# Kernel tuning notes

Measured on AMD Instinct MI355X. Metric: run time of the kernel, lower is better.

## Reference

```python
import jax, jax.numpy as jnp
import numpy as np

S, N_PER, N_FEAT, HID = 4, 12500, 1024, 256
N_STRUCT = 500


def setup_inputs() -> dict:
    key = jax.random.key(0)
    ks = jax.random.split(key, 11)
    sc = 1.0 / np.sqrt(N_FEAT)
    sh = 1.0 / np.sqrt(HID)
    return {
        "features": jax.random.normal(ks[0], (S, N_PER, N_FEAT), jnp.float32),
        "W1": jax.random.normal(ks[1], (S, N_FEAT, HID), jnp.float32) * sc,
        "b1": jax.random.normal(ks[2], (S, HID), jnp.float32) * 0.01,
        "W2": jax.random.normal(ks[3], (S, HID, HID), jnp.float32) * sh,
        "b2": jax.random.normal(ks[4], (S, HID), jnp.float32) * 0.01,
        "W3": jax.random.normal(ks[5], (S, HID, HID), jnp.float32) * sh,
        "b3": jax.random.normal(ks[6], (S, HID), jnp.float32) * 0.01,
        "W4": jax.random.normal(ks[7], (S, HID, 1), jnp.float32) * sh,
        "b4": jax.random.normal(ks[8], (S, 1), jnp.float32) * 0.01,
        "structure_idx": jax.random.randint(ks[9], (S, N_PER), 0, N_STRUCT, jnp.int64 if jax.config.jax_enable_x64 else jnp.int32).astype(jnp.int32),
        "n_structures": N_STRUCT,
    }


def reference(features, W1, b1, W2, b2, W3, b3, W4, b4, structure_idx, n_structures):
    # Per-species 4-layer SiLU MLP applied to species-grouped feature blocks.
    h = jax.nn.silu(jnp.einsum("snf,sfh->snh", features, W1) + b1[:, None, :])
    h = jax.nn.silu(jnp.einsum("snh,shk->snk", h, W2) + b2[:, None, :])
    h = jax.nn.silu(jnp.einsum("snh,shk->snk", h, W3) + b3[:, None, :])
    e = jnp.einsum("snh,sho->sno", h, W4) + b4[:, None, :]  # [S, N_per, 1]
    atomic_energies = e[..., 0].reshape(-1)                  # concat over species
    # index_add_ into per-structure energies
    energies = jax.ops.segment_sum(atomic_energies, structure_idx.reshape(-1), num_segments=n_structures)
    return energies
```

## Files before the change

### kernel.cpp

```cpp
#include <hip/hip_runtime.h>

typedef _Float16 f16;
typedef __attribute__((ext_vector_type(8))) _Float16 f16x8;
typedef __attribute__((ext_vector_type(4))) float f32x4;
typedef unsigned int u32;

#define S_      4
#define NPER    12500
#define NF      1024
#define HID     256
#define NSTRUCT 500
#define TM      64

#define GLB __attribute__((address_space(1)))
#define AS3 __attribute__((address_space(3)))

#define WAIT_VM(N)  asm volatile("s_waitcnt vmcnt(" #N ")" ::: "memory")
#define WAIT_LGKM() asm volatile("s_waitcnt lgkmcnt(0)" ::: "memory")
#define SCHED0()    __builtin_amdgcn_sched_barrier(0)
#define BARRIER()   do { __builtin_amdgcn_s_barrier(); SCHED0(); } while (0)

__global__ __launch_bounds__(256) void transpose_all_kernel(
    const float* __restrict__ W1, const float* __restrict__ W2,
    const float* __restrict__ W3,
    f16* __restrict__ w1t, f16* __restrict__ w2t, f16* __restrict__ w3t)
{
  const int z = blockIdx.z;
  const int layer = z >> 2, sp = z & 3;
  const float* in; f16* out; int K;
  if (layer == 0)      { in = W1; out = w1t; K = NF;  }
  else if (layer == 1) { in = W2; out = w2t; K = HID; }
  else                 { in = W3; out = w3t; K = HID; }
  if (blockIdx.x * 64 >= K) return;

  __shared__ float tile[64][65];
  const float* inp = in + (size_t)sp * K * HID;
  f16* outp = out + (size_t)sp * K * HID;
  const int k0 = blockIdx.x * 64;
  const int n0 = blockIdx.y * 64;
  const int t = threadIdx.x;
  {
    const int lk = t >> 2;
    const int nq = (t & 3) * 16;
    const float* src = inp + (size_t)(k0 + lk) * HID + n0 + nq;
    #pragma unroll
    for (int i = 0; i < 4; ++i) {
      float4 v = *(const float4*)(src + i * 4);
      tile[lk][nq + i * 4 + 0] = v.x;
      tile[lk][nq + i * 4 + 1] = v.y;
      tile[lk][nq + i * 4 + 2] = v.z;
      tile[lk][nq + i * 4 + 3] = v.w;
    }
  }
  __syncthreads();
  {
    const int ln = t >> 2;
    const int kq = (t & 3) * 16;
    f16* dst = outp + (size_t)(n0 + ln) * K + k0 + kq;
    f16x8 a, b;
    #pragma unroll
    for (int j = 0; j < 8; ++j) a[j] = (f16)tile[kq + j][ln];
    #pragma unroll
    for (int j = 0; j < 8; ++j) b[j] = (f16)tile[kq + 8 + j][ln];
    *(f16x8*)dst = a;
    *(f16x8*)(dst + 8) = b;
  }
}


__device__ __forceinline__ void zero_acc(f32x4 (&acc)[4][4]) {
  #pragma unroll
  for (int a = 0; a < 4; ++a)
    #pragma unroll
    for (int b = 0; b < 4; ++b)
      #pragma unroll
      for (int j = 0; j < 4; ++j) acc[a][b][j] = 0.f;
}

__device__ __forceinline__ void stage_w64(char* bS, const char* wbase, int c,
                                          int w, int lane)
{
  #pragma unroll
  for (int i = 0; i < 8; ++i) {
    const int seg  = w * 8 + i;
    const int rloc = lane >> 3;
    const int p    = lane & 7;
    const int row  = seg * 8 + rloc;
    const int slog = p ^ rloc;
    const char* gp = wbase + (size_t)row * (NF * 2) + (size_t)c * 128 + slog * 16;
    char* lp = bS + seg * 1024;
    __builtin_amdgcn_global_load_lds((const GLB u32*)gp, (AS3 u32*)lp, 16, 0, 0);
  }
}

__device__ __forceinline__ void stage_w32(char* wS, const char* wbase, int c,
                                          int w, int lane)
{
  #pragma unroll
  for (int i = 0; i < 4; ++i) {
    const int seg = w * 4 + i;
    const int row = seg * 16 + (lane >> 2);
    const int kbp = lane & 3;
    const int kb  = kbp ^ ((row >> 1) & 3);
    const char* gp = wbase + (size_t)row * (HID * 2) + c * 64 + kb * 16;
    char* lp = wS + seg * 1024;
    __builtin_amdgcn_global_load_lds((const GLB u32*)gp, (AS3 u32*)lp, 16, 0, 0);
  }
}

__device__ __forceinline__ void load_pa(float4 (&pa)[4], const float* fsrcT, int c)
{
  #pragma unroll
  for (int j = 0; j < 4; ++j)
    pa[j] = *(const float4*)(fsrcT + c * 64 + j * 4);
}

__device__ __forceinline__ void stage_feat64(char* aS, const float4 (&pa)[4], int t)
{
  const int r = t >> 2;
  #pragma unroll
  for (int wr = 0; wr < 2; ++wr) {
    f16x8 hv;
    const float4 lo = pa[wr * 2 + 0], hi = pa[wr * 2 + 1];
    hv[0]=(f16)lo.x; hv[1]=(f16)lo.y; hv[2]=(f16)lo.z; hv[3]=(f16)lo.w;
    hv[4]=(f16)hi.x; hv[5]=(f16)hi.y; hv[6]=(f16)hi.z; hv[7]=(f16)hi.w;
    const int slog = (t & 3) * 2 + wr;
    const int p = slog ^ (r & 7);
    *(f16x8*)(aS + r * 128 + p * 16) = hv;
  }
}

__device__ __forceinline__ void mfma64_a(f32x4 (&acc)[4][4], const char* aS,
                                         const char* bS, int w, int g, int l15)
{
  #pragma unroll
  for (int ks = 0; ks < 2; ++ks) {
    f16x8 af[4], bf[4];
    #pragma unroll
    for (int at = 0; at < 4; ++at) {
      const int rr = at * 16 + l15;
      const int p  = (ks * 4 + g) ^ (rr & 7);
      af[at] = *(const f16x8*)(aS + rr * 128 + p * 16);
    }
    #pragma unroll
    for (int bt = 0; bt < 4; ++bt) {
      const int nn = w * 64 + bt * 16 + l15;
      const int p  = (ks * 4 + g) ^ (nn & 7);
      bf[bt] = *(const f16x8*)(bS + nn * 128 + p * 16);
    }
    #pragma unroll
    for (int at = 0; at < 4; ++at)
      #pragma unroll
      for (int bt = 0; bt < 4; ++bt)
        acc[at][bt] = __builtin_amdgcn_mfma_f32_16x16x32_f16(af[at], bf[bt], acc[at][bt], 0, 0, 0);
  }
}

__device__ __forceinline__ void mfma32_h(f32x4 (&acc)[4][4], const char* hL, int c,
                                         const char* wS, int w, int g, int l15)
{
  f16x8 af[4], bf[4];
  #pragma unroll
  for (int at = 0; at < 4; ++at) {
    const int rr = at * 16 + l15;
    af[at] = *(const f16x8*)(hL + ((rr * 512 + c * 64 + g * 16) ^ ((rr & 7) << 4)));
  }
  #pragma unroll
  for (int bt = 0; bt < 4; ++bt) {
    const int nn = w * 64 + bt * 16 + l15;
    bf[bt] = *(const f16x8*)(wS + nn * 64 + ((g ^ ((nn >> 1) & 3)) * 16));
  }
  #pragma unroll
  for (int at = 0; at < 4; ++at)
    #pragma unroll
    for (int bt = 0; bt < 4; ++bt)
      acc[at][bt] = __builtin_amdgcn_mfma_f32_16x16x32_f16(af[at], bf[bt], acc[at][bt], 0, 0, 0);
}

__device__ __forceinline__ void silu_store(f32x4 (&acc)[4][4],
                                           const float* __restrict__ bias,
                                           char* hL, int w, int lane)
{
  const int g = lane >> 4, l15 = lane & 15;
  #pragma unroll
  for (int bt = 0; bt < 4; ++bt) {
    const int col = w * 64 + bt * 16 + l15;
    const float b = bias[col];
    #pragma unroll
    for (int at = 0; at < 4; ++at) {
      #pragma unroll
      for (int j = 0; j < 4; ++j) {
        const int row = at * 16 + g * 4 + j;
        float x = acc[at][bt][j] + b;
        x = x * __builtin_amdgcn_rcpf(1.f + __expf(-x));
        *(f16*)(hL + (((row * HID + col) * 2) ^ ((row & 7) << 4))) = (f16)x;
      }
    }
  }
}

#define L1_STEP(c, ASc, ASn, BSc, BSn, PAset, VMN, DOF, DOG, DOPA)  \
  do {                                                               \
    if (DOF)  stage_feat64(ASn, PAset, t);                           \
    if (DOG)  stage_w64(BSn, w1s, (c) + 1, w, lane);                 \
    if (DOPA) load_pa(PAset, fsrcT, (c) + 3);                        \
    WAIT_VM(VMN); SCHED0();                                          \
    mfma64_a(acc, ASc, BSc, w, g, l15);                              \
    WAIT_LGKM(); BARRIER();                                          \
  } while (0)

#define HID_NB(c, WSc, WSn, wsrc, DOG)                               \
  do {                                                               \
    WAIT_LGKM(); SCHED0();                                           \
    if (DOG) stage_w32(WSn, wsrc, (c) + 1, w, lane);                 \
    WAIT_VM(4); SCHED0();                                            \
    mfma32_h(acc, hL, c, WSc, w, g, l15);                            \
  } while (0)

__global__ __launch_bounds__(256, 2) void mlp_fused_kernel(
    const float* __restrict__ feats,
    const float* __restrict__ b1g,
    const float* __restrict__ b2g,
    const float* __restrict__ b3g,
    const float* __restrict__ w4g,
    const float* __restrict__ b4g,
    const int*   __restrict__ sidxg,
    const f16*   __restrict__ w1t,
    const f16*   __restrict__ w2t,
    const f16*   __restrict__ w3t,
    float*       __restrict__ outg)
{
  __shared__ char arena[80 * 1024];
  char* aS0 = arena;
  char* aS1 = arena + 8 * 1024;
  char* bS0 = arena + 16 * 1024;
  char* bS1 = arena + 48 * 1024;
  char* hL  = arena;
  char* wS0 = arena + 32 * 1024;
  char* wS1 = arena + 48 * 1024;

  const int s    = blockIdx.y;
  const int row0 = blockIdx.x * TM;
  const int t    = threadIdx.x;
  const int lane = t & 63;
  const int w    = t >> 6;
  const int g    = lane >> 4;
  const int l15  = lane & 15;

  const int gr   = row0 + (t >> 2);
  const bool valid = gr < NPER;
  const int grc  = valid ? gr : (NPER - 1);
  const float* fsrcT = feats + ((size_t)s * NPER + grc) * NF + (t & 3) * 16;
  const char*  w1s   = (const char*)(w1t + (size_t)s * HID * NF);
  const char*  w2s   = (const char*)(w2t + (size_t)s * HID * HID);
  const char*  w3s   = (const char*)(w3t + (size_t)s * HID * HID);

  f32x4 acc[4][4];
  zero_acc(acc);

  float4 pf[4], paA[4], paB[4];
  load_pa(pf, fsrcT, 0);
  stage_w64(bS0, w1s, 0, w, lane);
  load_pa(paA, fsrcT, 1);
  load_pa(paB, fsrcT, 2);
  stage_feat64(aS0, pf, t);
  WAIT_LGKM(); BARRIER();

  L1_STEP(0, aS0, aS1, bS0, bS1, paA, 20, 1, 1, 1);
  for (int cc = 1; cc <= 11; cc += 2) {
    L1_STEP(cc,     aS1, aS0, bS1, bS0, paB, 16, 1, 1, 1);
    L1_STEP(cc + 1, aS0, aS1, bS0, bS1, paA, 16, 1, 1, 1);
  }
  L1_STEP(13, aS1, aS0, bS1, bS0, paB, 12, 1, 1, 0);
  L1_STEP(14, aS0, aS1, bS0, bS1, paA,  8, 1, 1, 0);
  {
    stage_w32(wS0, w2s, 0, w, lane);
    WAIT_VM(4); SCHED0();
    mfma64_a(acc, aS1, bS1, w, g, l15);
    WAIT_LGKM(); BARRIER();
  }

  silu_store(acc, b1g + s * HID, hL, w, lane);
  zero_acc(acc);
  WAIT_LGKM(); BARRIER();

  HID_NB(0, wS0, wS1, w2s, 1);
  HID_NB(1, wS1, wS0, w2s, 1);
  HID_NB(2, wS0, wS1, w2s, 1);
  HID_NB(3, wS1, wS0, w2s, 1);
  HID_NB(4, wS0, wS1, w2s, 1);
  HID_NB(5, wS1, wS0, w2s, 1);
  HID_NB(6, wS0, wS1, w2s, 1);
  {
    WAIT_LGKM(); SCHED0();
    stage_w32(wS0, w3s, 0, w, lane);
    WAIT_VM(4); SCHED0();
    mfma32_h(acc, hL, 7, wS1, w, g, l15);
  }
  BARRIER();
  silu_store(acc, b2g + s * HID, hL, w, lane);
  zero_acc(acc);
  WAIT_LGKM(); BARRIER();

  HID_NB(0, wS0, wS1, w3s, 1);
  HID_NB(1, wS1, wS0, w3s, 1);
  HID_NB(2, wS0, wS1, w3s, 1);
  HID_NB(3, wS1, wS0, w3s, 1);
  HID_NB(4, wS0, wS1, w3s, 1);
  HID_NB(5, wS1, wS0, w3s, 1);
  HID_NB(6, wS0, wS1, w3s, 1);
  {
    WAIT_VM(0); SCHED0();
    mfma32_h(acc, hL, 7, wS1, w, g, l15);
  }
  BARRIER();
  silu_store(acc, b3g + s * HID, hL, w, lane);
  WAIT_LGKM(); BARRIER();

  {
    const int row = t >> 2;
    const int q   = t & 3;
    const float* w4 = w4g + s * HID;
    float sum = 0.f;
    #pragma unroll
    for (int j8 = 0; j8 < 64; j8 += 8) {
      const int k = q * 64 + j8;
      f16x8 hv = *(const f16x8*)(hL + (((row * HID + k) * 2) ^ ((row & 7) << 4)));
      float4 wa = *(const float4*)(w4 + k);
      float4 wb = *(const float4*)(w4 + k + 4);
      sum += (float)hv[0] * wa.x + (float)hv[1] * wa.y + (float)hv[2] * wa.z + (float)hv[3] * wa.w
           + (float)hv[4] * wb.x + (float)hv[5] * wb.y + (float)hv[6] * wb.z + (float)hv[7] * wb.w;
    }
    sum += __shfl_xor(sum, 1);
    sum += __shfl_xor(sum, 2);
    if (q == 0 && valid) {
      atomicAdd(&outg[sidxg[s * NPER + gr]], sum + b4g[s]);
    }
  }
}

extern "C" void kernel_launch(void* const* d_in, const int* in_sizes, int n_in,
                              void* d_out, int out_size, void* d_ws, size_t ws_size,
                              hipStream_t stream)
{
  const float* feats = (const float*)d_in[0];
  const float* W1    = (const float*)d_in[1];
  const float* b1    = (const float*)d_in[2];
  const float* W2    = (const float*)d_in[3];
  const float* b2    = (const float*)d_in[4];
  const float* W3    = (const float*)d_in[5];
  const float* b3    = (const float*)d_in[6];
  const float* W4    = (const float*)d_in[7];
  const float* b4    = (const float*)d_in[8];
  const int*   sidx  = (const int*)d_in[9];
  float* out = (float*)d_out;

  f16* w1t = (f16*)d_ws;
  f16* w2t = w1t + (size_t)S_ * HID * NF;
  f16* w3t = w2t + (size_t)S_ * HID * HID;

  hipMemsetAsync(d_out, 0, NSTRUCT * sizeof(float), stream);
  transpose_all_kernel<<<dim3(16, 4, 12), 256, 0, stream>>>(W1, W2, W3, w1t, w2t, w3t);
  mlp_fused_kernel<<<dim3((NPER + TM - 1) / TM, S_), 256, 0, stream>>>(
      feats, b1, b2, b3, W4, b4, sidx, w1t, w2t, w3t, out);
}
```

Before: 110.1 us.

## Stage fp32 features via direct LDS loads and keep weight tiles in registers

Features are now copied straight from global memory into LDS as fp32 with async global_load_lds into a triple buffer, and converted to fp16 only when the MFMA operands are read. Weight tiles for all three layers are loaded from global memory directly into registers, double-buffered, instead of being staged in LDS. This shrinks LDS from 80KB to 48KB so three blocks can share a CU, and removes the register round-trip and conversion stores for features. In exchange, LDS traffic per feature element doubles, register pressure rises, and the hidden layers issue global weight loads without explicit waits, relying on the compiler to insert them.

```diff
diff --git a/kernel.cpp b/kernel.cpp
--- a/kernel.cpp
+++ b/kernel.cpp
@@ -77,104 +77,76 @@
       for (int j = 0; j < 4; ++j) acc[a][b][j] = 0.f;
 }
 
-__device__ __forceinline__ void stage_w64(char* bS, const char* wbase, int c,
-                                          int w, int lane)
-{
-  #pragma unroll
-  for (int i = 0; i < 8; ++i) {
-    const int seg  = w * 8 + i;
-    const int rloc = lane >> 3;
-    const int p    = lane & 7;
-    const int row  = seg * 8 + rloc;
-    const int slog = p ^ rloc;
-    const char* gp = wbase + (size_t)row * (NF * 2) + (size_t)c * 128 + slog * 16;
-    char* lp = bS + seg * 1024;
+__device__ __forceinline__ void stage_a64(char* aS, const float* fbase, int c,
+                                          int row0, int w, int lane)
+{
+  #pragma unroll
+  for (int i = 0; i < 4; ++i) {
+    const int row  = i * 16 + w * 4 + (lane >> 4);
+    const int p    = lane & 15;
+    const int slog = p ^ (row & 15);
+    int rg = row0 + row; if (rg > NPER - 1) rg = NPER - 1;
+    const float* gp = fbase + (size_t)rg * NF + c * 64 + slog * 4;
+    char* lp = aS + ((i * 16 + w * 4) << 8);
     __builtin_amdgcn_global_load_lds((const GLB u32*)gp, (AS3 u32*)lp, 16, 0, 0);
   }
 }
 
-__device__ __forceinline__ void stage_w32(char* wS, const char* wbase, int c,
-                                          int w, int lane)
-{
-  #pragma unroll
-  for (int i = 0; i < 4; ++i) {
-    const int seg = w * 4 + i;
-    const int row = seg * 16 + (lane >> 2);
-    const int kbp = lane & 3;
-    const int kb  = kbp ^ ((row >> 1) & 3);
-    const char* gp = wbase + (size_t)row * (HID * 2) + c * 64 + kb * 16;
-    char* lp = wS + seg * 1024;
-    __builtin_amdgcn_global_load_lds((const GLB u32*)gp, (AS3 u32*)lp, 16, 0, 0);
-  }
-}
-
-__device__ __forceinline__ void load_pa(float4 (&pa)[4], const float* fsrcT, int c)
-{
-  #pragma unroll
-  for (int j = 0; j < 4; ++j)
-    pa[j] = *(const float4*)(fsrcT + c * 64 + j * 4);
-}
-
-__device__ __forceinline__ void stage_feat64(char* aS, const float4 (&pa)[4], int t)
-{
-  const int r = t >> 2;
-  #pragma unroll
-  for (int wr = 0; wr < 2; ++wr) {
-    f16x8 hv;
-    const float4 lo = pa[wr * 2 + 0], hi = pa[wr * 2 + 1];
-    hv[0]=(f16)lo.x; hv[1]=(f16)lo.y; hv[2]=(f16)lo.z; hv[3]=(f16)lo.w;
-    hv[4]=(f16)hi.x; hv[5]=(f16)hi.y; hv[6]=(f16)hi.z; hv[7]=(f16)hi.w;
-    const int slog = (t & 3) * 2 + wr;
-    const int p = slog ^ (r & 7);
-    *(f16x8*)(aS + r * 128 + p * 16) = hv;
-  }
-}
-
-__device__ __forceinline__ void mfma64_a(f32x4 (&acc)[4][4], const char* aS,
-                                         const char* bS, int w, int g, int l15)
+__device__ __forceinline__ void load_b64(f16x8 (&bf)[8], const f16* wsrc, int c,
+                                         int K, int w, int g, int l15)
+{
+  #pragma unroll
+  for (int ks = 0; ks < 2; ++ks)
+    #pragma unroll
+    for (int bt = 0; bt < 4; ++bt) {
+      const int nn = w * 64 + bt * 16 + l15;
+      bf[ks * 4 + bt] = *(const f16x8*)(wsrc + (size_t)nn * K + c * 64 + (ks * 4 + g) * 8);
+    }
+}
+
+__device__ __forceinline__ void mfma64_f32a(f32x4 (&acc)[4][4], const char* aS,
+                                            const f16x8 (&bf)[8], int g, int l15)
 {
   #pragma unroll
   for (int ks = 0; ks < 2; ++ks) {
-    f16x8 af[4], bf[4];
+    f16x8 af[4];
     #pragma unroll
     for (int at = 0; at < 4; ++at) {
       const int rr = at * 16 + l15;
-      const int p  = (ks * 4 + g) ^ (rr & 7);
-      af[at] = *(const f16x8*)(aS + rr * 128 + p * 16);
-    }
-    #pragma unroll
-    for (int bt = 0; bt < 4; ++bt) {
-      const int nn = w * 64 + bt * 16 + l15;
-      const int p  = (ks * 4 + g) ^ (nn & 7);
-      bf[bt] = *(const f16x8*)(bS + nn * 128 + p * 16);
+      const int sw = rr & 15;
+      const int s0 = ks * 8 + g * 2;
+      const f32x4 lo = *(const f32x4*)(aS + rr * 256 + ((s0    ) ^ sw) * 16);
+      const f32x4 hi = *(const f32x4*)(aS + rr * 256 + ((s0 + 1) ^ sw) * 16);
+      f16x8 a;
+      a[0]=(f16)lo[0]; a[1]=(f16)lo[1]; a[2]=(f16)lo[2]; a[3]=(f16)lo[3];
+      a[4]=(f16)hi[0]; a[5]=(f16)hi[1]; a[6]=(f16)hi[2]; a[7]=(f16)hi[3];
+      af[at] = a;
     }
     #pragma unroll
     for (int at = 0; at < 4; ++at)
       #pragma unroll
       for (int bt = 0; bt < 4; ++bt)
-        acc[at][bt] = __builtin_amdgcn_mfma_f32_16x16x32_f16(af[at], bf[bt], acc[at][bt], 0, 0, 0);
-  }
-}
-
-__device__ __forceinline__ void mfma32_h(f32x4 (&acc)[4][4], const char* hL, int c,
-                                         const char* wS, int w, int g, int l15)
-{
-  f16x8 af[4], bf[4];
-  #pragma unroll
-  for (int at = 0; at < 4; ++at) {
-    const int rr = at * 16 + l15;
-    af[at] = *(const f16x8*)(hL + ((rr * 512 + c * 64 + g * 16) ^ ((rr & 7) << 4)));
-  }
-  #pragma unroll
-  for (int bt = 0; bt < 4; ++bt) {
-    const int nn = w * 64 + bt * 16 + l15;
-    bf[bt] = *(const f16x8*)(wS + nn * 64 + ((g ^ ((nn >> 1) & 3)) * 16));
-  }
-  #pragma unroll
-  for (int at = 0; at < 4; ++at)
-    #pragma unroll
-    for (int bt = 0; bt < 4; ++bt)
-      acc[at][bt] = __builtin_amdgcn_mfma_f32_16x16x32_f16(af[at], bf[bt], acc[at][bt], 0, 0, 0);
+        acc[at][bt] = __builtin_amdgcn_mfma_f32_16x16x32_f16(af[at], bf[ks*4+bt], acc[at][bt], 0, 0, 0);
+  }
+}
+
+__device__ __forceinline__ void mfma64_h(f32x4 (&acc)[4][4], const char* hL, int cH,
+                                         const f16x8 (&bf)[8], int g, int l15)
+{
+  #pragma unroll
+  for (int ks = 0; ks < 2; ++ks) {
+    f16x8 af[4];
+    #pragma unroll
+    for (int at = 0; at < 4; ++at) {
+      const int rr = at * 16 + l15;
+      af[at] = *(const f16x8*)(hL + ((rr * 512 + cH * 128 + ks * 64 + g * 16) ^ ((rr & 7) << 4)));
+    }
+    #pragma unroll
+    for (int at = 0; at < 4; ++at)
+      #pragma unroll
+      for (int bt = 0; bt < 4; ++bt)
+        acc[at][bt] = __builtin_amdgcn_mfma_f32_16x16x32_f16(af[at], bf[ks*4+bt], acc[at][bt], 0, 0, 0);
+  }
 }
 
 __device__ __forceinline__ void silu_store(f32x4 (&acc)[4][4],
@@ -199,25 +171,16 @@
   }
 }
 
-#define L1_STEP(c, ASc, ASn, BSc, BSn, PAset, VMN, DOF, DOG, DOPA)  \
-  do {                                                               \
-    if (DOF)  stage_feat64(ASn, PAset, t);                           \
-    if (DOG)  stage_w64(BSn, w1s, (c) + 1, w, lane);                 \
-    if (DOPA) load_pa(PAset, fsrcT, (c) + 3);                        \
-    WAIT_VM(VMN); SCHED0();                                          \
-    mfma64_a(acc, ASc, BSc, w, g, l15);                              \
-    WAIT_LGKM(); BARRIER();                                          \
+#define L1_PH(c, AScur, ASstg, BFcur, BFnxt, DOA, DOB, VMN)   \
+  do {                                                         \
+    if (DOA) stage_a64(ASstg, fbase, (c) + 2, row0, w, lane);  \
+    if (DOB) load_b64(BFnxt, w1s, (c) + 1, NF, w, g, l15);     \
+    WAIT_VM(VMN); SCHED0();                                    \
+    mfma64_f32a(acc, AScur, BFcur, g, l15);                    \
+    WAIT_LGKM(); BARRIER();                                    \
   } while (0)
 
-#define HID_NB(c, WSc, WSn, wsrc, DOG)                               \
-  do {                                                               \
-    WAIT_LGKM(); SCHED0();                                           \
-    if (DOG) stage_w32(WSn, wsrc, (c) + 1, w, lane);                 \
-    WAIT_VM(4); SCHED0();                                            \
-    mfma32_h(acc, hL, c, WSc, w, g, l15);                            \
-  } while (0)
-
-__global__ __launch_bounds__(256, 2) void mlp_fused_kernel(
+__global__ __launch_bounds__(256, 3) void mlp_fused_kernel(
     const float* __restrict__ feats,
     const float* __restrict__ b1g,
     const float* __restrict__ b2g,
@@ -230,14 +193,11 @@
     const f16*   __restrict__ w3t,
     float*       __restrict__ outg)
 {
-  __shared__ char arena[80 * 1024];
+  __shared__ char arena[48 * 1024];
   char* aS0 = arena;
-  char* aS1 = arena + 8 * 1024;
-  char* bS0 = arena + 16 * 1024;
-  char* bS1 = arena + 48 * 1024;
+  char* aS1 = arena + 16 * 1024;
+  char* aS2 = arena + 32 * 1024;
   char* hL  = arena;
-  char* wS0 = arena + 32 * 1024;
-  char* wS1 = arena + 48 * 1024;
 
   const int s    = blockIdx.y;
   const int row0 = blockIdx.x * TM;
@@ -250,33 +210,40 @@
   const int gr   = row0 + (t >> 2);
   const bool valid = gr < NPER;
   const int grc  = valid ? gr : (NPER - 1);
-  const float* fsrcT = feats + ((size_t)s * NPER + grc) * NF + (t & 3) * 16;
-  const char*  w1s   = (const char*)(w1t + (size_t)s * HID * NF);
-  const char*  w2s   = (const char*)(w2t + (size_t)s * HID * HID);
-  const char*  w3s   = (const char*)(w3t + (size_t)s * HID * HID);
+  const float* fbase = feats + (size_t)s * NPER * NF;
+  const f16*   w1s   = w1t + (size_t)s * HID * NF;
+  const f16*   w2s   = w2t + (size_t)s * HID * HID;
+  const f16*   w3s   = w3t + (size_t)s * HID * HID;
 
   f32x4 acc[4][4];
+  f16x8 bfA[8], bfB[8];
   zero_acc(acc);
 
-  float4 pf[4], paA[4], paB[4];
-  load_pa(pf, fsrcT, 0);
-  stage_w64(bS0, w1s, 0, w, lane);
-  load_pa(paA, fsrcT, 1);
-  load_pa(paB, fsrcT, 2);
-  stage_feat64(aS0, pf, t);
-  WAIT_LGKM(); BARRIER();
-
-  L1_STEP(0, aS0, aS1, bS0, bS1, paA, 20, 1, 1, 1);
-  for (int cc = 1; cc <= 11; cc += 2) {
-    L1_STEP(cc,     aS1, aS0, bS1, bS0, paB, 16, 1, 1, 1);
-    L1_STEP(cc + 1, aS0, aS1, bS0, bS1, paA, 16, 1, 1, 1);
-  }
-  L1_STEP(13, aS1, aS0, bS1, bS0, paB, 12, 1, 1, 0);
-  L1_STEP(14, aS0, aS1, bS0, bS1, paA,  8, 1, 1, 0);
+  stage_a64(aS0, fbase, 0, row0, w, lane);
+  stage_a64(aS1, fbase, 1, row0, w, lane);
+  load_b64(bfA, w1s, 0, NF, w, g, l15);
+  WAIT_VM(12); SCHED0();
+  BARRIER();
+
+  L1_PH(0,  aS0, aS2, bfA, bfB, 1, 1, 12);
+  L1_PH(1,  aS1, aS0, bfB, bfA, 1, 1, 12);
+  L1_PH(2,  aS2, aS1, bfA, bfB, 1, 1, 12);
+  L1_PH(3,  aS0, aS2, bfB, bfA, 1, 1, 12);
+  L1_PH(4,  aS1, aS0, bfA, bfB, 1, 1, 12);
+  L1_PH(5,  aS2, aS1, bfB, bfA, 1, 1, 12);
+  L1_PH(6,  aS0, aS2, bfA, bfB, 1, 1, 12);
+  L1_PH(7,  aS1, aS0, bfB, bfA, 1, 1, 12);
+  L1_PH(8,  aS2, aS1, bfA, bfB, 1, 1, 12);
+  L1_PH(9,  aS0, aS2, bfB, bfA, 1, 1, 12);
+  L1_PH(10, aS1, aS0, bfA, bfB, 1, 1, 12);
+  L1_PH(11, aS2, aS1, bfB, bfA, 1, 1, 12);
+  L1_PH(12, aS0, aS2, bfA, bfB, 1, 1, 12);
+  L1_PH(13, aS1, aS0, bfB, bfA, 1, 1, 12);
+  L1_PH(14, aS2, aS0, bfA, bfB, 0, 1, 8);
   {
-    stage_w32(wS0, w2s, 0, w, lane);
-    WAIT_VM(4); SCHED0();
-    mfma64_a(acc, aS1, bS1, w, g, l15);
+    WAIT_VM(0); SCHED0();
+    mfma64_f32a(acc, aS0, bfB, g, l15);
+    load_b64(bfA, w2s, 0, HID, w, g, l15);
     WAIT_LGKM(); BARRIER();
   }
 
@@ -284,35 +251,26 @@
   zero_acc(acc);
   WAIT_LGKM(); BARRIER();
 
-  HID_NB(0, wS0, wS1, w2s, 1);
-  HID_NB(1, wS1, wS0, w2s, 1);
-  HID_NB(2, wS0, wS1, w2s, 1);
-  HID_NB(3, wS1, wS0, w2s, 1);
-  HID_NB(4, wS0, wS1, w2s, 1);
-  HID_NB(5, wS1, wS0, w2s, 1);
-  HID_NB(6, wS0, wS1, w2s, 1);
-  {
-    WAIT_LGKM(); SCHED0();
-    stage_w32(wS0, w3s, 0, w, lane);
-    WAIT_VM(4); SCHED0();
-    mfma32_h(acc, hL, 7, wS1, w, g, l15);
-  }
+  load_b64(bfB, w2s, 1, HID, w, g, l15);
+  mfma64_h(acc, hL, 0, bfA, g, l15);
+  load_b64(bfA, w2s, 2, HID, w, g, l15);
+  mfma64_h(acc, hL, 1, bfB, g, l15);
+  load_b64(bfB, w2s, 3, HID, w, g, l15);
+  mfma64_h(acc, hL, 2, bfA, g, l15);
+  load_b64(bfA, w3s, 0, HID, w, g, l15);
+  mfma64_h(acc, hL, 3, bfB, g, l15);
   BARRIER();
   silu_store(acc, b2g + s * HID, hL, w, lane);
   zero_acc(acc);
   WAIT_LGKM(); BARRIER();
 
-  HID_NB(0, wS0, wS1, w3s, 1);
-  HID_NB(1, wS1, wS0, w3s, 1);
-  HID_NB(2, wS0, wS1, w3s, 1);
-  HID_NB(3, wS1, wS0, w3s, 1);
-  HID_NB(4, wS0, wS1, w3s, 1);
-  HID_NB(5, wS1, wS0, w3s, 1);
-  HID_NB(6, wS0, wS1, w3s, 1);
-  {
-    WAIT_VM(0); SCHED0();
-    mfma32_h(acc, hL, 7, wS1, w, g, l15);
-  }
+  load_b64(bfB, w3s, 1, HID, w, g, l15);
+  mfma64_h(acc, hL, 0, bfA, g, l15);
+  load_b64(bfA, w3s, 2, HID, w, g, l15);
+  mfma64_h(acc, hL, 1, bfB, g, l15);
+  load_b64(bfB, w3s, 3, HID, w, g, l15);
+  mfma64_h(acc, hL, 2, bfA, g, l15);
+  mfma64_h(acc, hL, 3, bfB, g, l15);
   BARRIER();
   silu_store(acc, b3g + s * HID, hL, w, lane);
   WAIT_LGKM(); BARRIER();
```

New measurement: 158.3 us. +43.8%, slower.

## Deepen prefetch pipelines: 4-stage feature loads and triple-buffered hidden weights

Applied to the files above, without the earlier changes.

Layer 1 now keeps three register prefetch sets for feature tiles, loading chunk c+4 instead of c+3, so global-load latency has more time to hide. The hidden layers switch from double to triple-buffered weight staging in LDS, using a third 16KB slot. The weights for layer 3 are prefetched across the layer boundary. This raises register pressure and keeps more loads in flight, and it relies on the per-wave waitcnt discipline staying correct without barriers between stages.

```diff
diff --git a/kernel.cpp b/kernel.cpp
--- a/kernel.cpp
+++ b/kernel.cpp
@@ -199,22 +199,22 @@
   }
 }
 
-#define L1_STEP(c, ASc, ASn, BSc, BSn, PAset, VMN, DOF, DOG, DOPA)  \
-  do {                                                               \
-    if (DOF)  stage_feat64(ASn, PAset, t);                           \
-    if (DOG)  stage_w64(BSn, w1s, (c) + 1, w, lane);                 \
-    if (DOPA) load_pa(PAset, fsrcT, (c) + 3);                        \
-    WAIT_VM(VMN); SCHED0();                                          \
-    mfma64_a(acc, ASc, BSc, w, g, l15);                              \
-    WAIT_LGKM(); BARRIER();                                          \
+#define L1_STEP(c, ASc, ASn, BSc, BSn, PAset, VMN, DOG, DOPA)   \
+  do {                                                           \
+    stage_feat64(ASn, PAset, t);                                 \
+    if (DOG)  stage_w64(BSn, w1s, (c) + 1, w, lane);             \
+    if (DOPA) load_pa(PAset, fsrcT, (c) + 4);                    \
+    WAIT_VM(VMN); SCHED0();                                      \
+    mfma64_a(acc, ASc, BSc, w, g, l15);                          \
+    WAIT_LGKM(); BARRIER();                                      \
   } while (0)
 
-#define HID_NB(c, WSc, WSn, wsrc, DOG)                               \
-  do {                                                               \
-    WAIT_LGKM(); SCHED0();                                           \
-    if (DOG) stage_w32(WSn, wsrc, (c) + 1, w, lane);                 \
-    WAIT_VM(4); SCHED0();                                            \
-    mfma32_h(acc, hL, c, WSc, w, g, l15);                            \
+#define HID_ST(c, WSc, WSstg, wsrc, cs)                          \
+  do {                                                           \
+    WAIT_VM(8); SCHED0();                                        \
+    mfma32_h(acc, hL, c, WSc, w, g, l15);                        \
+    WAIT_LGKM(); SCHED0();                                       \
+    stage_w32(WSstg, wsrc, cs, w, lane);                         \
   } while (0)
 
 __global__ __launch_bounds__(256, 2) void mlp_fused_kernel(
@@ -238,6 +238,7 @@
   char* hL  = arena;
   char* wS0 = arena + 32 * 1024;
   char* wS1 = arena + 48 * 1024;
+  char* wS2 = arena + 64 * 1024;
 
   const int s    = blockIdx.y;
   const int row0 = blockIdx.x * TM;
@@ -258,21 +259,30 @@
   f32x4 acc[4][4];
   zero_acc(acc);
 
-  float4 pf[4], paA[4], paB[4];
+  float4 pf[4], paA[4], paB[4], paC[4];
   load_pa(pf, fsrcT, 0);
   stage_w64(bS0, w1s, 0, w, lane);
   load_pa(paA, fsrcT, 1);
   load_pa(paB, fsrcT, 2);
+  load_pa(paC, fsrcT, 3);
   stage_feat64(aS0, pf, t);
   WAIT_LGKM(); BARRIER();
 
-  L1_STEP(0, aS0, aS1, bS0, bS1, paA, 20, 1, 1, 1);
-  for (int cc = 1; cc <= 11; cc += 2) {
-    L1_STEP(cc,     aS1, aS0, bS1, bS0, paB, 16, 1, 1, 1);
-    L1_STEP(cc + 1, aS0, aS1, bS0, bS1, paA, 16, 1, 1, 1);
-  }
-  L1_STEP(13, aS1, aS0, bS1, bS0, paB, 12, 1, 1, 0);
-  L1_STEP(14, aS0, aS1, bS0, bS1, paA,  8, 1, 1, 0);
+  L1_STEP(0,  aS0, aS1, bS0, bS1, paA, 20, 1, 1);
+  L1_STEP(1,  aS1, aS0, bS1, bS0, paB, 16, 1, 1);
+  L1_STEP(2,  aS0, aS1, bS0, bS1, paC, 16, 1, 1);
+  L1_STEP(3,  aS1, aS0, bS1, bS0, paA, 16, 1, 1);
+  L1_STEP(4,  aS0, aS1, bS0, bS1, paB, 16, 1, 1);
+  L1_STEP(5,  aS1, aS0, bS1, bS0, paC, 16, 1, 1);
+  L1_STEP(6,  aS0, aS1, bS0, bS1, paA, 16, 1, 1);
+  L1_STEP(7,  aS1, aS0, bS1, bS0, paB, 16, 1, 1);
+  L1_STEP(8,  aS0, aS1, bS0, bS1, paC, 16, 1, 1);
+  L1_STEP(9,  aS1, aS0, bS1, bS0, paA, 16, 1, 1);
+  L1_STEP(10, aS0, aS1, bS0, bS1, paB, 16, 1, 1);
+  L1_STEP(11, aS1, aS0, bS1, bS0, paC, 16, 1, 1);
+  L1_STEP(12, aS0, aS1, bS0, bS1, paA, 12, 1, 0);
+  L1_STEP(13, aS1, aS0, bS1, bS0, paB,  8, 1, 0);
+  L1_STEP(14, aS0, aS1, bS0, bS1, paC,  8, 1, 0);
   {
     stage_w32(wS0, w2s, 0, w, lane);
     WAIT_VM(4); SCHED0();
@@ -282,37 +292,31 @@
 
   silu_store(acc, b1g + s * HID, hL, w, lane);
   zero_acc(acc);
+  stage_w32(wS1, w2s, 1, w, lane);
+  stage_w32(wS2, w2s, 2, w, lane);
   WAIT_LGKM(); BARRIER();
 
-  HID_NB(0, wS0, wS1, w2s, 1);
-  HID_NB(1, wS1, wS0, w2s, 1);
-  HID_NB(2, wS0, wS1, w2s, 1);
-  HID_NB(3, wS1, wS0, w2s, 1);
-  HID_NB(4, wS0, wS1, w2s, 1);
-  HID_NB(5, wS1, wS0, w2s, 1);
-  HID_NB(6, wS0, wS1, w2s, 1);
-  {
-    WAIT_LGKM(); SCHED0();
-    stage_w32(wS0, w3s, 0, w, lane);
-    WAIT_VM(4); SCHED0();
-    mfma32_h(acc, hL, 7, wS1, w, g, l15);
-  }
+  HID_ST(0, wS0, wS0, w2s, 3);
+  HID_ST(1, wS1, wS1, w2s, 4);
+  HID_ST(2, wS2, wS2, w2s, 5);
+  HID_ST(3, wS0, wS0, w2s, 6);
+  HID_ST(4, wS1, wS1, w2s, 7);
+  HID_ST(5, wS2, wS2, w3s, 0);
+  HID_ST(6, wS0, wS0, w3s, 1);
+  HID_ST(7, wS1, wS1, w3s, 2);
   BARRIER();
   silu_store(acc, b2g + s * HID, hL, w, lane);
   zero_acc(acc);
   WAIT_LGKM(); BARRIER();
 
-  HID_NB(0, wS0, wS1, w3s, 1);
-  HID_NB(1, wS1, wS0, w3s, 1);
-  HID_NB(2, wS0, wS1, w3s, 1);
-  HID_NB(3, wS1, wS0, w3s, 1);
-  HID_NB(4, wS0, wS1, w3s, 1);
-  HID_NB(5, wS1, wS0, w3s, 1);
-  HID_NB(6, wS0, wS1, w3s, 1);
-  {
-    WAIT_VM(0); SCHED0();
-    mfma32_h(acc, hL, 7, wS1, w, g, l15);
-  }
+  HID_ST(0, wS2, wS2, w3s, 3);
+  HID_ST(1, wS0, wS0, w3s, 4);
+  HID_ST(2, wS1, wS1, w3s, 5);
+  HID_ST(3, wS2, wS2, w3s, 6);
+  HID_ST(4, wS0, wS0, w3s, 7);
+  { WAIT_VM(8); SCHED0(); mfma32_h(acc, hL, 5, wS1, w, g, l15); }
+  { WAIT_VM(4); SCHED0(); mfma32_h(acc, hL, 6, wS2, w, g, l15); }
+  { WAIT_VM(0); SCHED0(); mfma32_h(acc, hL, 7, wS0, w, g, l15); }
   BARRIER();
   silu_store(acc, b3g + s * HID, hL, w, lane);
   WAIT_LGKM(); BARRIER();
```

After: 108.3 us. No clear change (-1.6%).

## Enlarge row tile to 96 and restructure LDS pipeline with 4-deep feature ring

Applied to the files above, without the earlier changes.

Raises the per-block row tile from 64 to 96 so each staged weight chunk is reused across more rows, reducing weight traffic per row and block count. Layer 1 switches to a four-slot feature ring in LDS with a single weight buffer and a barrier every two steps. The hidden layers prefetch two weight chunks ahead, including across the layer boundary. More accumulator registers (6x4 tiles) may pressure occupancy at 2 blocks/CU, and the LDS reuse pattern relies on careful wait counts.

```diff
diff --git a/kernel.cpp b/kernel.cpp
--- a/kernel.cpp
+++ b/kernel.cpp
@@ -10,7 +10,7 @@
 #define NF      1024
 #define HID     256
 #define NSTRUCT 500
-#define TM      64
+#define TM      96
 
 #define GLB __attribute__((address_space(1)))
 #define AS3 __attribute__((address_space(3)))
@@ -68,9 +68,9 @@
 }
 
 
-__device__ __forceinline__ void zero_acc(f32x4 (&acc)[4][4]) {
-  #pragma unroll
-  for (int a = 0; a < 4; ++a)
+__device__ __forceinline__ void zero_acc(f32x4 (&acc)[6][4]) {
+  #pragma unroll
+  for (int a = 0; a < 6; ++a)
     #pragma unroll
     for (int b = 0; b < 4; ++b)
       #pragma unroll
@@ -108,36 +108,37 @@
   }
 }
 
-__device__ __forceinline__ void load_pa(float4 (&pa)[4], const float* fsrcT, int c)
-{
-  #pragma unroll
-  for (int j = 0; j < 4; ++j)
-    pa[j] = *(const float4*)(fsrcT + c * 64 + j * 4);
-}
-
-__device__ __forceinline__ void stage_feat64(char* aS, const float4 (&pa)[4], int t)
-{
-  const int r = t >> 2;
-  #pragma unroll
-  for (int wr = 0; wr < 2; ++wr) {
+__device__ __forceinline__ void load_pa96(float4 (&pa)[6],
+                                          const float* const (&agp)[3], int c)
+{
+  #pragma unroll
+  for (int i = 0; i < 3; ++i) {
+    pa[2*i]   = *(const float4*)(agp[i] + (size_t)c * 64);
+    pa[2*i+1] = *(const float4*)(agp[i] + (size_t)c * 64 + 4);
+  }
+}
+
+__device__ __forceinline__ void stage_feat96(char* aS, const float4 (&pa)[6],
+                                             const u32 (&aof)[3])
+{
+  #pragma unroll
+  for (int i = 0; i < 3; ++i) {
     f16x8 hv;
-    const float4 lo = pa[wr * 2 + 0], hi = pa[wr * 2 + 1];
+    const float4 lo = pa[2*i], hi = pa[2*i+1];
     hv[0]=(f16)lo.x; hv[1]=(f16)lo.y; hv[2]=(f16)lo.z; hv[3]=(f16)lo.w;
     hv[4]=(f16)hi.x; hv[5]=(f16)hi.y; hv[6]=(f16)hi.z; hv[7]=(f16)hi.w;
-    const int slog = (t & 3) * 2 + wr;
-    const int p = slog ^ (r & 7);
-    *(f16x8*)(aS + r * 128 + p * 16) = hv;
-  }
-}
-
-__device__ __forceinline__ void mfma64_a(f32x4 (&acc)[4][4], const char* aS,
+    *(f16x8*)(aS + aof[i]) = hv;
+  }
+}
+
+__device__ __forceinline__ void mfma96_a(f32x4 (&acc)[6][4], const char* aS,
                                          const char* bS, int w, int g, int l15)
 {
   #pragma unroll
   for (int ks = 0; ks < 2; ++ks) {
-    f16x8 af[4], bf[4];
-    #pragma unroll
-    for (int at = 0; at < 4; ++at) {
+    f16x8 af[6], bf[4];
+    #pragma unroll
+    for (int at = 0; at < 6; ++at) {
       const int rr = at * 16 + l15;
       const int p  = (ks * 4 + g) ^ (rr & 7);
       af[at] = *(const f16x8*)(aS + rr * 128 + p * 16);
@@ -149,19 +150,19 @@
       bf[bt] = *(const f16x8*)(bS + nn * 128 + p * 16);
     }
     #pragma unroll
-    for (int at = 0; at < 4; ++at)
+    for (int at = 0; at < 6; ++at)
       #pragma unroll
       for (int bt = 0; bt < 4; ++bt)
         acc[at][bt] = __builtin_amdgcn_mfma_f32_16x16x32_f16(af[at], bf[bt], acc[at][bt], 0, 0, 0);
   }
 }
 
-__device__ __forceinline__ void mfma32_h(f32x4 (&acc)[4][4], const char* hL, int c,
+__device__ __forceinline__ void mfma32_h(f32x4 (&acc)[6][4], const char* hL, int c,
                                          const char* wS, int w, int g, int l15)
 {
-  f16x8 af[4], bf[4];
-  #pragma unroll
-  for (int at = 0; at < 4; ++at) {
+  f16x8 af[6], bf[4];
+  #pragma unroll
+  for (int at = 0; at < 6; ++at) {
     const int rr = at * 16 + l15;
     af[at] = *(const f16x8*)(hL + ((rr * 512 + c * 64 + g * 16) ^ ((rr & 7) << 4)));
   }
@@ -171,13 +172,13 @@
     bf[bt] = *(const f16x8*)(wS + nn * 64 + ((g ^ ((nn >> 1) & 3)) * 16));
   }
   #pragma unroll
-  for (int at = 0; at < 4; ++at)
+  for (int at = 0; at < 6; ++at)
     #pragma unroll
     for (int bt = 0; bt < 4; ++bt)
       acc[at][bt] = __builtin_amdgcn_mfma_f32_16x16x32_f16(af[at], bf[bt], acc[at][bt], 0, 0, 0);
 }
 
-__device__ __forceinline__ void silu_store(f32x4 (&acc)[4][4],
+__device__ __forceinline__ void silu_store(f32x4 (&acc)[6][4],
                                            const float* __restrict__ bias,
                                            char* hL, int w, int lane)
 {
@@ -187,7 +188,7 @@
     const int col = w * 64 + bt * 16 + l15;
     const float b = bias[col];
     #pragma unroll
-    for (int at = 0; at < 4; ++at) {
+    for (int at = 0; at < 6; ++at) {
       #pragma unroll
       for (int j = 0; j < 4; ++j) {
         const int row = at * 16 + g * 4 + j;
@@ -199,22 +200,25 @@
   }
 }
 
-#define L1_STEP(c, ASc, ASn, BSc, BSn, PAset, VMN, DOF, DOG, DOPA)  \
-  do {                                                               \
-    if (DOF)  stage_feat64(ASn, PAset, t);                           \
-    if (DOG)  stage_w64(BSn, w1s, (c) + 1, w, lane);                 \
-    if (DOPA) load_pa(PAset, fsrcT, (c) + 3);                        \
-    WAIT_VM(VMN); SCHED0();                                          \
-    mfma64_a(acc, ASc, BSc, w, g, l15);                              \
-    WAIT_LGKM(); BARRIER();                                          \
+#define ASB(c) (arena + (((c) & 3) * 12288))
+
+#define L1_STEP(c, PAset, VMN, DOG, DOF, DOPA, DOBAR)              \
+  do {                                                             \
+    WAIT_VM(VMN); SCHED0();                                        \
+    mfma96_a(acc, ASB(c), bS, w, g, l15);                          \
+    WAIT_LGKM(); SCHED0();                                         \
+    if (DOG)  { stage_w64(bS, w1s, (c) + 1, w, lane); SCHED0(); }  \
+    if (DOF)  { stage_feat96(ASB((c) + 2), PAset, aof); SCHED0(); }\
+    if (DOPA) { load_pa96(PAset, agp, (c) + 4); SCHED0(); }        \
+    if (DOBAR) { WAIT_LGKM(); BARRIER(); }                         \
   } while (0)
 
-#define HID_NB(c, WSc, WSn, wsrc, DOG)                               \
-  do {                                                               \
-    WAIT_LGKM(); SCHED0();                                           \
-    if (DOG) stage_w32(WSn, wsrc, (c) + 1, w, lane);                 \
-    WAIT_VM(4); SCHED0();                                            \
-    mfma32_h(acc, hL, c, WSc, w, g, l15);                            \
+#define HID_ST(c, WH, wsrc, cs)                                  \
+  do {                                                           \
+    WAIT_VM(4); SCHED0();                                        \
+    mfma32_h(acc, hL, c, WH, w, g, l15);                         \
+    WAIT_LGKM(); SCHED0();                                       \
+    stage_w32(WH, wsrc, cs, w, lane); SCHED0();                  \
   } while (0)
 
 __global__ __launch_bounds__(256, 2) void mlp_fused_kernel(
@@ -231,13 +235,10 @@
     float*       __restrict__ outg)
 {
   __shared__ char arena[80 * 1024];
-  char* aS0 = arena;
-  char* aS1 = arena + 8 * 1024;
-  char* bS0 = arena + 16 * 1024;
-  char* bS1 = arena + 48 * 1024;
+  char* bS  = arena + 48 * 1024;
   char* hL  = arena;
-  char* wS0 = arena + 32 * 1024;
-  char* wS1 = arena + 48 * 1024;
+  char* wH0 = arena + 48 * 1024;
+  char* wH1 = arena + 64 * 1024;
 
   const int s    = blockIdx.y;
   const int row0 = blockIdx.x * TM;
@@ -247,94 +248,107 @@
   const int g    = lane >> 4;
   const int l15  = lane & 15;
 
-  const int gr   = row0 + (t >> 2);
-  const bool valid = gr < NPER;
-  const int grc  = valid ? gr : (NPER - 1);
-  const float* fsrcT = feats + ((size_t)s * NPER + grc) * NF + (t & 3) * 16;
+  const float* fbase = feats + (size_t)s * NPER * NF;
   const char*  w1s   = (const char*)(w1t + (size_t)s * HID * NF);
   const char*  w2s   = (const char*)(w2t + (size_t)s * HID * HID);
   const char*  w3s   = (const char*)(w3t + (size_t)s * HID * HID);
 
-  f32x4 acc[4][4];
+  const int sl = t & 7;
+  const float* agp[3];
+  u32 aof[3];
+  #pragma unroll
+  for (int i = 0; i < 3; ++i) {
+    const int rw = (t + 256 * i) >> 3;
+    int rg = row0 + rw; if (rg > NPER - 1) rg = NPER - 1;
+    agp[i] = fbase + (size_t)rg * NF + sl * 8;
+    aof[i] = (u32)(rw * 128 + ((sl ^ (rw & 7)) << 4));
+  }
+
+  f32x4 acc[6][4];
+
+  float4 pf0[6], pf1[6], paA[6], paB[6];
+  load_pa96(pf0, agp, 0);  SCHED0();
+  load_pa96(pf1, agp, 1);  SCHED0();
+  stage_w64(bS, w1s, 0, w, lane);  SCHED0();
+  load_pa96(paA, agp, 2);  SCHED0();
+  load_pa96(paB, agp, 3);  SCHED0();
+  stage_feat96(ASB(0), pf0, aof);  SCHED0();
+  stage_feat96(ASB(1), pf1, aof);  SCHED0();
   zero_acc(acc);
-
-  float4 pf[4], paA[4], paB[4];
-  load_pa(pf, fsrcT, 0);
-  stage_w64(bS0, w1s, 0, w, lane);
-  load_pa(paA, fsrcT, 1);
-  load_pa(paB, fsrcT, 2);
-  stage_feat64(aS0, pf, t);
   WAIT_LGKM(); BARRIER();
 
-  L1_STEP(0, aS0, aS1, bS0, bS1, paA, 20, 1, 1, 1);
-  for (int cc = 1; cc <= 11; cc += 2) {
-    L1_STEP(cc,     aS1, aS0, bS1, bS0, paB, 16, 1, 1, 1);
-    L1_STEP(cc + 1, aS0, aS1, bS0, bS1, paA, 16, 1, 1, 1);
-  }
-  L1_STEP(13, aS1, aS0, bS1, bS0, paB, 12, 1, 1, 0);
-  L1_STEP(14, aS0, aS1, bS0, bS1, paA,  8, 1, 1, 0);
+  L1_STEP(0,  paA, 12, 1, 1, 1, 0);
+  L1_STEP(1,  paB,  6, 1, 1, 1, 1);
+  L1_STEP(2,  paA,  6, 1, 1, 1, 0);
+  L1_STEP(3,  paB,  6, 1, 1, 1, 1);
+  L1_STEP(4,  paA,  6, 1, 1, 1, 0);
+  L1_STEP(5,  paB,  6, 1, 1, 1, 1);
+  L1_STEP(6,  paA,  6, 1, 1, 1, 0);
+  L1_STEP(7,  paB,  6, 1, 1, 1, 1);
+  L1_STEP(8,  paA,  6, 1, 1, 1, 0);
+  L1_STEP(9,  paB,  6, 1, 1, 1, 1);
+  L1_STEP(10, paA,  6, 1, 1, 1, 0);
+  L1_STEP(11, paB,  6, 1, 1, 1, 1);
+  L1_STEP(12, paA,  6, 1, 1, 0, 0);
+  L1_STEP(13, paB,  0, 1, 1, 0, 1);
+  L1_STEP(14, paA,  0, 1, 0, 0, 0);
   {
-    stage_w32(wS0, w2s, 0, w, lane);
-    WAIT_VM(4); SCHED0();
-    mfma64_a(acc, aS1, bS1, w, g, l15);
+    WAIT_VM(0); SCHED0();
+    mfma96_a(acc, ASB(15), bS, w, g, l15);
     WAIT_LGKM(); BARRIER();
   }
 
+  stage_w32(wH0, w2s, 0, w, lane);  SCHED0();
+  stage_w32(wH1, w2s, 1, w, lane);  SCHED0();
   silu_store(acc, b1g + s * HID, hL, w, lane);
   zero_acc(acc);
   WAIT_LGKM(); BARRIER();
 
-  HID_NB(0, wS0, wS1, w2s, 1);
-  HID_NB(1, wS1, wS0, w2s, 1);
-  HID_NB(2, wS0, wS1, w2s, 1);
-  HID_NB(3, wS1, wS0, w2s, 1);
-  HID_NB(4, wS0, wS1, w2s, 1);
-  HID_NB(5, wS1, wS0, w2s, 1);
-  HID_NB(6, wS0, wS1, w2s, 1);
-  {
-    WAIT_LGKM(); SCHED0();
-    stage_w32(wS0, w3s, 0, w, lane);
-    WAIT_VM(4); SCHED0();
-    mfma32_h(acc, hL, 7, wS1, w, g, l15);
-  }
+  HID_ST(0, wH0, w2s, 2);
+  HID_ST(1, wH1, w2s, 3);
+  HID_ST(2, wH0, w2s, 4);
+  HID_ST(3, wH1, w2s, 5);
+  HID_ST(4, wH0, w2s, 6);
+  HID_ST(5, wH1, w2s, 7);
+  HID_ST(6, wH0, w3s, 0);
+  HID_ST(7, wH1, w3s, 1);
   BARRIER();
   silu_store(acc, b2g + s * HID, hL, w, lane);
   zero_acc(acc);
   WAIT_LGKM(); BARRIER();
 
-  HID_NB(0, wS0, wS1, w3s, 1);
-  HID_NB(1, wS1, wS0, w3s, 1);
-  HID_NB(2, wS0, wS1, w3s, 1);
-  HID_NB(3, wS1, wS0, w3s, 1);
-  HID_NB(4, wS0, wS1, w3s, 1);
-  HID_NB(5, wS1, wS0, w3s, 1);
-  HID_NB(6, wS0, wS1, w3s, 1);
-  {
-    WAIT_VM(0); SCHED0();
-    mfma32_h(acc, hL, 7, wS1, w, g, l15);
-  }
+  HID_ST(0, wH0, w3s, 2);
+  HID_ST(1, wH1, w3s, 3);
+  HID_ST(2, wH0, w3s, 4);
+  HID_ST(3, wH1, w3s, 5);
+  HID_ST(4, wH0, w3s, 6);
+  HID_ST(5, wH1, w3s, 7);
+  { WAIT_VM(4); SCHED0(); mfma32_h(acc, hL, 6, wH0, w, g, l15); }
+  { WAIT_VM(0); SCHED0(); mfma32_h(acc, hL, 7, wH1, w, g, l15); }
   BARRIER();
   silu_store(acc, b3g + s * HID, hL, w, lane);
   WAIT_LGKM(); BARRIER();
 
   {
-    const int row = t >> 2;
-    const int q   = t & 3;
-    const float* w4 = w4g + s * HID;
-    float sum = 0.f;
-    #pragma unroll
-    for (int j8 = 0; j8 < 64; j8 += 8) {
-      const int k = q * 64 + j8;
-      f16x8 hv = *(const f16x8*)(hL + (((row * HID + k) * 2) ^ ((row & 7) << 4)));
-      float4 wa = *(const float4*)(w4 + k);
-      float4 wb = *(const float4*)(w4 + k + 4);
-      sum += (float)hv[0] * wa.x + (float)hv[1] * wa.y + (float)hv[2] * wa.z + (float)hv[3] * wa.w
-           + (float)hv[4] * wb.x + (float)hv[5] * wb.y + (float)hv[6] * wb.z + (float)hv[7] * wb.w;
-    }
-    sum += __shfl_xor(sum, 1);
-    sum += __shfl_xor(sum, 2);
-    if (q == 0 && valid) {
-      atomicAdd(&outg[sidxg[s * NPER + gr]], sum + b4g[s]);
+    const int row = t >> 1;
+    const int q   = t & 1;
+    if (row < TM) {
+      const int grL = row0 + row;
+      const float* w4 = w4g + s * HID;
+      float sum = 0.f;
+      #pragma unroll
+      for (int j8 = 0; j8 < 128; j8 += 8) {
+        const int k = q * 128 + j8;
+        f16x8 hv = *(const f16x8*)(hL + (((row * HID + k) * 2) ^ ((row & 7) << 4)));
+        float4 wa = *(const float4*)(w4 + k);
+        float4 wb = *(const float4*)(w4 + k + 4);
+        sum += (float)hv[0] * wa.x + (float)hv[1] * wa.y + (float)hv[2] * wa.z + (float)hv[3] * wa.w
+             + (float)hv[4] * wb.x + (float)hv[5] * wb.y + (float)hv[6] * wb.z + (float)hv[7] * wb.w;
+      }
+      sum += __shfl_xor(sum, 1);
+      if (q == 0 && grL < NPER) {
+        atomicAdd(&outg[sidxg[s * NPER + grL]], sum + b4g[s]);
+      }
     }
   }
 }
```

Result: slower. 138.3 us (+25.6%).
